# Performance work log

Measured on AMD Instinct MI355X. Metric: run time of the kernel, lower is better.

Reference implementation:

```python
import jax, jax.numpy as jnp
import numpy as np

EPS = 1e-6


def setup_inputs() -> dict:
    key = jax.random.key(0)
    k1, k2, k3 = jax.random.split(key, 3)
    N, D, C = 65536, 512, 1000
    x = jax.random.normal(k1, (N, D), dtype=jnp.float32)
    # learned class centers (rows ~ unit-ish scale like the orthogonal init)
    weight = jax.random.normal(k2, (C, D), dtype=jnp.float32) / np.sqrt(D)
    targets = jax.random.randint(k3, (N,), 0, C)
    return {"x": x, "weight": weight, "targets": targets}


def reference(x, weight, targets):
    # Original computes full [N, C] euclidean distances then gathers only the
    # target entry per row via onehot+nonzero. Mathematically identical (and
    # exact, not an approximation) is gathering the target center per sample
    # and computing its distance directly.
    w_t = weight[targets]                               # [N, D] gather by class
    d = jnp.sqrt(jnp.sum((x - w_t) ** 2, axis=1) + EPS)  # [N]
    return jnp.mean(d)
```

## Files before the change

kernel.cpp:

```cpp
#include <hip/hip_runtime.h>


constexpr int D = 512;
constexpr float EPS = 1e-6f;

__global__ __launch_bounds__(256) void centerloss_kernel(
    const float* __restrict__ x,
    const float* __restrict__ w,
    const int*   __restrict__ targets,
    float* __restrict__ out,
    int n_rows)
{
    const int lane = threadIdx.x & 63;
    const int wave = threadIdx.x >> 6;
    const int wavesPerBlock = blockDim.x >> 6;
    const int globalWave = blockIdx.x * wavesPerBlock + wave;
    const int waveCount = gridDim.x * wavesPerBlock;

    float wsum = 0.0f;

    for (int row = globalWave; row < n_rows; row += waveCount) {
        const int t = targets[row];
        const float4* __restrict__ xr =
            reinterpret_cast<const float4*>(x + (size_t)row * D);
        const float4* __restrict__ wr =
            reinterpret_cast<const float4*>(w + (size_t)t * D);

        float4 xa = xr[lane];
        float4 wa = wr[lane];
        float4 xb = xr[lane + 64];
        float4 wb = wr[lane + 64];

        float acc = 0.0f, d0;
        d0 = xa.x - wa.x; acc = fmaf(d0, d0, acc);
        d0 = xa.y - wa.y; acc = fmaf(d0, d0, acc);
        d0 = xa.z - wa.z; acc = fmaf(d0, d0, acc);
        d0 = xa.w - wa.w; acc = fmaf(d0, d0, acc);
        d0 = xb.x - wb.x; acc = fmaf(d0, d0, acc);
        d0 = xb.y - wb.y; acc = fmaf(d0, d0, acc);
        d0 = xb.z - wb.z; acc = fmaf(d0, d0, acc);
        d0 = xb.w - wb.w; acc = fmaf(d0, d0, acc);

        #pragma unroll
        for (int off = 1; off < 64; off <<= 1)
            acc += __shfl_xor(acc, off, 64);

        wsum += sqrtf(acc + EPS);
    }

    __shared__ float smem[8];
    if (lane == 0) smem[wave] = wsum;
    __syncthreads();

    if (threadIdx.x == 0) {
        float s = 0.0f;
        for (int i = 0; i < wavesPerBlock; ++i) s += smem[i];
        atomicAdd(out, s * (1.0f / (float)n_rows));
    }
}

extern "C" void kernel_launch(void* const* d_in, const int* in_sizes, int n_in,
                              void* d_out, int out_size, void* d_ws, size_t ws_size,
                              hipStream_t stream) {
    const float* x       = (const float*)d_in[0];
    const float* weight  = (const float*)d_in[1];
    const int*   targets = (const int*)d_in[2];
    float* out = (float*)d_out;

    const int n_rows = in_sizes[2];

    hipMemsetAsync(d_out, 0, sizeof(float), stream);

    const int block = 256;
    const int grid  = 2048;
    centerloss_kernel<<<grid, block, 0, stream>>>(x, weight, targets, out, n_rows);
}
```

Before: 206.8 us.

## Process contiguous rows per wave with batched target loads and nontemporal x reads

Each wave now owns a contiguous block of 8 rows, loads their targets with one vector load and broadcasts them via readlane, and processes two rows per iteration so more loads are in flight. Loads of x use nontemporal hints so they bypass cache retention, leaving cache for the weight rows, which are reused. The grid is sized to cover every row exactly once instead of using a fixed grid-stride loop, which increases the block count and the number of atomics.

Measured after the change: 200.1 us. -3.2%, faster.

```diff
diff --git a/kernel.cpp b/kernel.cpp
--- a/kernel.cpp
+++ b/kernel.cpp
@@ -1,61 +1,100 @@
 #include <hip/hip_runtime.h>
 
 
+typedef float f32x4 __attribute__((ext_vector_type(4)));
+
 constexpr int D = 512;
 constexpr float EPS = 1e-6f;
+constexpr int RPW = 8;
+constexpr int WPB = 4;
 
 __global__ __launch_bounds__(256) void centerloss_kernel(
     const float* __restrict__ x,
     const float* __restrict__ w,
     const int*   __restrict__ targets,
     float* __restrict__ out,
-    int n_rows)
+    int n_rows, float inv_n)
 {
     const int lane = threadIdx.x & 63;
     const int wave = threadIdx.x >> 6;
-    const int wavesPerBlock = blockDim.x >> 6;
-    const int globalWave = blockIdx.x * wavesPerBlock + wave;
-    const int waveCount = gridDim.x * wavesPerBlock;
+    const int gw = blockIdx.x * WPB + wave;
+    const long base = (long)gw * RPW;
+
+    int tml = 0;
+    {
+        const long r = base + lane;
+        if (lane < RPW && r < (long)n_rows) tml = targets[r];
+    }
 
     float wsum = 0.0f;
+    const f32x4 fz = {0.f, 0.f, 0.f, 0.f};
 
-    for (int row = globalWave; row < n_rows; row += waveCount) {
-        const int t = targets[row];
-        const float4* __restrict__ xr =
-            reinterpret_cast<const float4*>(x + (size_t)row * D);
-        const float4* __restrict__ wr =
-            reinterpret_cast<const float4*>(w + (size_t)t * D);
+    #pragma unroll
+    for (int k = 0; k < RPW; k += 2) {
+        const long r0 = base + k;
+        const long r1 = base + k + 1;
+        const bool v0 = r0 < (long)n_rows;
+        const bool v1 = r1 < (long)n_rows;
+        const int t0 = __builtin_amdgcn_readlane(tml, k);
+        const int t1 = __builtin_amdgcn_readlane(tml, k + 1);
 
-        float4 xa = xr[lane];
-        float4 wa = wr[lane];
-        float4 xb = xr[lane + 64];
-        float4 wb = wr[lane + 64];
+        const f32x4* __restrict__ xr0 = reinterpret_cast<const f32x4*>(x + r0 * D);
+        const f32x4* __restrict__ xr1 = reinterpret_cast<const f32x4*>(x + r1 * D);
+        const f32x4* __restrict__ wr0 = reinterpret_cast<const f32x4*>(w + (size_t)t0 * D);
+        const f32x4* __restrict__ wr1 = reinterpret_cast<const f32x4*>(w + (size_t)t1 * D);
 
-        float acc = 0.0f, d0;
-        d0 = xa.x - wa.x; acc = fmaf(d0, d0, acc);
-        d0 = xa.y - wa.y; acc = fmaf(d0, d0, acc);
-        d0 = xa.z - wa.z; acc = fmaf(d0, d0, acc);
-        d0 = xa.w - wa.w; acc = fmaf(d0, d0, acc);
-        d0 = xb.x - wb.x; acc = fmaf(d0, d0, acc);
-        d0 = xb.y - wb.y; acc = fmaf(d0, d0, acc);
-        d0 = xb.z - wb.z; acc = fmaf(d0, d0, acc);
-        d0 = xb.w - wb.w; acc = fmaf(d0, d0, acc);
+        f32x4 xa0 = fz, xb0 = fz, wa0 = fz, wb0 = fz;
+        f32x4 xa1 = fz, xb1 = fz, wa1 = fz, wb1 = fz;
+        if (v0) {
+            xa0 = __builtin_nontemporal_load(&xr0[lane]);
+            xb0 = __builtin_nontemporal_load(&xr0[lane + 64]);
+            wa0 = wr0[lane];
+            wb0 = wr0[lane + 64];
+        }
+        if (v1) {
+            xa1 = __builtin_nontemporal_load(&xr1[lane]);
+            xb1 = __builtin_nontemporal_load(&xr1[lane + 64]);
+            wa1 = wr1[lane];
+            wb1 = wr1[lane + 64];
+        }
+
+        float a0 = 0.f, a1 = 0.f, d;
+        d = xa0.x - wa0.x; a0 = fmaf(d, d, a0);
+        d = xa0.y - wa0.y; a0 = fmaf(d, d, a0);
+        d = xa0.z - wa0.z; a0 = fmaf(d, d, a0);
+        d = xa0.w - wa0.w; a0 = fmaf(d, d, a0);
+        d = xb0.x - wb0.x; a0 = fmaf(d, d, a0);
+        d = xb0.y - wb0.y; a0 = fmaf(d, d, a0);
+        d = xb0.z - wb0.z; a0 = fmaf(d, d, a0);
+        d = xb0.w - wb0.w; a0 = fmaf(d, d, a0);
+
+        d = xa1.x - wa1.x; a1 = fmaf(d, d, a1);
+        d = xa1.y - wa1.y; a1 = fmaf(d, d, a1);
+        d = xa1.z - wa1.z; a1 = fmaf(d, d, a1);
+        d = xa1.w - wa1.w; a1 = fmaf(d, d, a1);
+        d = xb1.x - wb1.x; a1 = fmaf(d, d, a1);
+        d = xb1.y - wb1.y; a1 = fmaf(d, d, a1);
+        d = xb1.z - wb1.z; a1 = fmaf(d, d, a1);
+        d = xb1.w - wb1.w; a1 = fmaf(d, d, a1);
 
         #pragma unroll
-        for (int off = 1; off < 64; off <<= 1)
-            acc += __shfl_xor(acc, off, 64);
-
-        wsum += sqrtf(acc + EPS);
+        for (int off = 1; off < 64; off <<= 1) {
+            a0 += __shfl_xor(a0, off, 64);
+            a1 += __shfl_xor(a1, off, 64);
+        }
+        if (v0) wsum += sqrtf(a0 + EPS);
+        if (v1) wsum += sqrtf(a1 + EPS);
     }
 
-    __shared__ float smem[8];
+    __shared__ float smem[WPB];
     if (lane == 0) smem[wave] = wsum;
     __syncthreads();
 
     if (threadIdx.x == 0) {
         float s = 0.0f;
-        for (int i = 0; i < wavesPerBlock; ++i) s += smem[i];
-        atomicAdd(out, s * (1.0f / (float)n_rows));
+        #pragma unroll
+        for (int i = 0; i < WPB; ++i) s += smem[i];
+        atomicAdd(out, s * inv_n);
     }
 }
 
@@ -69,9 +108,10 @@
 
     const int n_rows = in_sizes[2];
 
-    hipMemsetAsync(d_out, 0, sizeof(float), stream);
+    (void)hipMemsetAsync(d_out, 0, sizeof(float), stream);
 
-    const int block = 256;
-    const int grid  = 2048;
-    centerloss_kernel<<<grid, block, 0, stream>>>(x, weight, targets, out, n_rows);
+    const int rowsPerBlock = WPB * RPW;
+    const int grid = (n_rows + rowsPerBlock - 1) / rowsPerBlock;
+    centerloss_kernel<<<grid, 256, 0, stream>>>(x, weight, targets, out,
+                                                n_rows, 1.0f / (float)n_rows);
 }
```

## Bucket rows by target class so each block reuses one center in registers

Applied to the files above, without the earlier changes.

Adds a counting-sort pipeline (count, scan, scatter) that groups row indices by target class. The main kernel then runs one block per class, loads that class's center once into registers, and streams the matching x rows with nontemporal loads while prefetching the next row index. The aim is to remove the repeated per-row gather of weight rows. In exchange it adds three extra launches and a memset, atomic contention on the class counters, and load imbalance across the 1000 class blocks. Reads of x become scattered rather than sequential.

After: 234.0 us. 1.13x slower.

```diff
diff --git a/kernel.cpp b/kernel.cpp
--- a/kernel.cpp
+++ b/kernel.cpp
@@ -1,61 +1,96 @@
 #include <hip/hip_runtime.h>
 
+
+typedef float f32x4 __attribute__((ext_vector_type(4)));
 
 constexpr int D = 512;
 constexpr float EPS = 1e-6f;
 
-__global__ __launch_bounds__(256) void centerloss_kernel(
-    const float* __restrict__ x,
-    const float* __restrict__ w,
-    const int*   __restrict__ targets,
-    float* __restrict__ out,
-    int n_rows)
+__global__ void k_count(const int* __restrict__ targets, int n,
+                        int* __restrict__ counts) {
+    int i = blockIdx.x * blockDim.x + threadIdx.x;
+    if (i < n) atomicAdd(&counts[targets[i]], 1);
+}
+
+__global__ __launch_bounds__(1024) void k_scan(const int* __restrict__ counts,
+                                               int* __restrict__ offsets,
+                                               int* __restrict__ cursors, int C) {
+    __shared__ int s[1024];
+    const int tid = threadIdx.x;
+    const int cnt = (tid < C) ? counts[tid] : 0;
+    s[tid] = cnt;
+    __syncthreads();
+    for (int off = 1; off < 1024; off <<= 1) {
+        int v = (tid >= off) ? s[tid - off] : 0;
+        __syncthreads();
+        s[tid] += v;
+        __syncthreads();
+    }
+    if (tid < C) {
+        const int excl = s[tid] - cnt;
+        offsets[tid] = excl;
+        cursors[tid] = excl;
+    }
+}
+
+__global__ void k_scatter(const int* __restrict__ targets, int n,
+                          int* __restrict__ cursors, int* __restrict__ bucket) {
+    int i = blockIdx.x * blockDim.x + threadIdx.x;
+    if (i < n) {
+        int pos = atomicAdd(&cursors[targets[i]], 1);
+        bucket[pos] = i;
+    }
+}
+
+__global__ __launch_bounds__(256) void k_main(
+    const float* __restrict__ x, const float* __restrict__ w,
+    const int* __restrict__ offsets, const int* __restrict__ counts,
+    const int* __restrict__ bucket, float* __restrict__ out, float inv_n)
 {
     const int lane = threadIdx.x & 63;
     const int wave = threadIdx.x >> 6;
-    const int wavesPerBlock = blockDim.x >> 6;
-    const int globalWave = blockIdx.x * wavesPerBlock + wave;
-    const int waveCount = gridDim.x * wavesPerBlock;
+    const int c = blockIdx.x;
+    const int start = offsets[c];
+    const int cnt   = counts[c];
+
+    const f32x4* __restrict__ wr = reinterpret_cast<const f32x4*>(w + (size_t)c * D);
+    const f32x4 wa = wr[lane];
+    const f32x4 wb = wr[lane + 64];
 
     float wsum = 0.0f;
 
-    for (int row = globalWave; row < n_rows; row += waveCount) {
-        const int t = targets[row];
-        const float4* __restrict__ xr =
-            reinterpret_cast<const float4*>(x + (size_t)row * D);
-        const float4* __restrict__ wr =
-            reinterpret_cast<const float4*>(w + (size_t)t * D);
+    int row = (wave < cnt) ? bucket[start + wave] : 0;
+    for (int j = wave; j < cnt; j += 4) {
+        const int nrow = (j + 4 < cnt) ? bucket[start + j + 4] : 0;
 
-        float4 xa = xr[lane];
-        float4 wa = wr[lane];
-        float4 xb = xr[lane + 64];
-        float4 wb = wr[lane + 64];
+        const f32x4* __restrict__ xr =
+            reinterpret_cast<const f32x4*>(x + (size_t)row * D);
+        const f32x4 xa = __builtin_nontemporal_load(&xr[lane]);
+        const f32x4 xb = __builtin_nontemporal_load(&xr[lane + 64]);
 
-        float acc = 0.0f, d0;
-        d0 = xa.x - wa.x; acc = fmaf(d0, d0, acc);
-        d0 = xa.y - wa.y; acc = fmaf(d0, d0, acc);
-        d0 = xa.z - wa.z; acc = fmaf(d0, d0, acc);
-        d0 = xa.w - wa.w; acc = fmaf(d0, d0, acc);
-        d0 = xb.x - wb.x; acc = fmaf(d0, d0, acc);
-        d0 = xb.y - wb.y; acc = fmaf(d0, d0, acc);
-        d0 = xb.z - wb.z; acc = fmaf(d0, d0, acc);
-        d0 = xb.w - wb.w; acc = fmaf(d0, d0, acc);
+        float a = 0.0f, d;
+        d = xa.x - wa.x; a = fmaf(d, d, a);
+        d = xa.y - wa.y; a = fmaf(d, d, a);
+        d = xa.z - wa.z; a = fmaf(d, d, a);
+        d = xa.w - wa.w; a = fmaf(d, d, a);
+        d = xb.x - wb.x; a = fmaf(d, d, a);
+        d = xb.y - wb.y; a = fmaf(d, d, a);
+        d = xb.z - wb.z; a = fmaf(d, d, a);
+        d = xb.w - wb.w; a = fmaf(d, d, a);
 
         #pragma unroll
         for (int off = 1; off < 64; off <<= 1)
-            acc += __shfl_xor(acc, off, 64);
+            a += __shfl_xor(a, off, 64);
 
-        wsum += sqrtf(acc + EPS);
+        wsum += sqrtf(a + EPS);
+        row = nrow;
     }
 
-    __shared__ float smem[8];
+    __shared__ float smem[4];
     if (lane == 0) smem[wave] = wsum;
     __syncthreads();
-
     if (threadIdx.x == 0) {
-        float s = 0.0f;
-        for (int i = 0; i < wavesPerBlock; ++i) s += smem[i];
-        atomicAdd(out, s * (1.0f / (float)n_rows));
+        atomicAdd(out, (smem[0] + smem[1] + smem[2] + smem[3]) * inv_n);
     }
 }
 
@@ -68,10 +103,22 @@
     float* out = (float*)d_out;
 
     const int n_rows = in_sizes[2];
+    const int C      = in_sizes[1] / D;
 
-    hipMemsetAsync(d_out, 0, sizeof(float), stream);
+    int* ws_i    = (int*)d_ws;
+    int* counts  = ws_i;
+    int* offsets = ws_i + 1024;
+    int* cursors = ws_i + 2048;
+    int* bucket  = ws_i + 3072;
 
-    const int block = 256;
-    const int grid  = 2048;
-    centerloss_kernel<<<grid, block, 0, stream>>>(x, weight, targets, out, n_rows);
+    (void)hipMemsetAsync(d_out, 0, sizeof(float), stream);
+    (void)hipMemsetAsync(counts, 0, 1024 * sizeof(int), stream);
+
+    const int tblk = 256;
+    const int tgrid = (n_rows + tblk - 1) / tblk;
+    k_count  <<<tgrid, tblk, 0, stream>>>(targets, n_rows, counts);
+    k_scan   <<<1, 1024, 0, stream>>>(counts, offsets, cursors, C);
+    k_scatter<<<tgrid, tblk, 0, stream>>>(targets, n_rows, cursors, bucket);
+    k_main   <<<C, 256, 0, stream>>>(x, weight, offsets, counts, bucket,
+                                     out, 1.0f / (float)n_rows);
 }
```

## Process four rows per wave with 16-lane groups and one-shot grid

Applied to the files above, without the earlier changes.

Each wave now owns a fixed chunk of 8 rows and splits into four 16-lane groups, each reducing one row per step with 8 vector loads per lane, so the cross-lane reduction shrinks to 4 shuffle stages. Targets are loaded once per wave and broadcast by shuffle. The grid-stride loop is replaced by one block per 32 rows, giving many more blocks and more loads in flight per lane. Because every lane in a group holds the full row sum, the wave total is 16 times too large, and the final scale divides by 16N to compensate. The cost is more blocks and more atomics on the output.

Result: slower. 213.8 us (+3.4%).

```diff
diff --git a/kernel.cpp b/kernel.cpp
--- a/kernel.cpp
+++ b/kernel.cpp
@@ -1,61 +1,80 @@
 #include <hip/hip_runtime.h>
 
 
+typedef float f32x4 __attribute__((ext_vector_type(4)));
+
 constexpr int D = 512;
 constexpr float EPS = 1e-6f;
+constexpr int RPW = 8;
+constexpr int WPB = 4;
 
 __global__ __launch_bounds__(256) void centerloss_kernel(
     const float* __restrict__ x,
     const float* __restrict__ w,
     const int*   __restrict__ targets,
     float* __restrict__ out,
-    int n_rows)
+    int n_rows, float inv_16n)
 {
     const int lane = threadIdx.x & 63;
     const int wave = threadIdx.x >> 6;
-    const int wavesPerBlock = blockDim.x >> 6;
-    const int globalWave = blockIdx.x * wavesPerBlock + wave;
-    const int waveCount = gridDim.x * wavesPerBlock;
+    const int grp  = lane >> 4;
+    const int sub  = lane & 15;
+    const int gw = blockIdx.x * WPB + wave;
+    const long base = (long)gw * RPW;
+
+    int tml = 0;
+    if (lane < RPW) {
+        const long r = base + lane;
+        if (r < (long)n_rows) tml = targets[r];
+    }
 
     float wsum = 0.0f;
+    const bool fast = (base + RPW) <= (long)n_rows;
 
-    for (int row = globalWave; row < n_rows; row += waveCount) {
-        const int t = targets[row];
-        const float4* __restrict__ xr =
-            reinterpret_cast<const float4*>(x + (size_t)row * D);
-        const float4* __restrict__ wr =
-            reinterpret_cast<const float4*>(w + (size_t)t * D);
+    #pragma unroll
+    for (int step = 0; step < 2; ++step) {
+        const long r = base + step * 4 + grp;
+        const int  t = __shfl(tml, step * 4 + grp, 64);
+        const bool v = fast || (r < (long)n_rows);
 
-        float4 xa = xr[lane];
-        float4 wa = wr[lane];
-        float4 xb = xr[lane + 64];
-        float4 wb = wr[lane + 64];
-
-        float acc = 0.0f, d0;
-        d0 = xa.x - wa.x; acc = fmaf(d0, d0, acc);
-        d0 = xa.y - wa.y; acc = fmaf(d0, d0, acc);
-        d0 = xa.z - wa.z; acc = fmaf(d0, d0, acc);
-        d0 = xa.w - wa.w; acc = fmaf(d0, d0, acc);
-        d0 = xb.x - wb.x; acc = fmaf(d0, d0, acc);
-        d0 = xb.y - wb.y; acc = fmaf(d0, d0, acc);
-        d0 = xb.z - wb.z; acc = fmaf(d0, d0, acc);
-        d0 = xb.w - wb.w; acc = fmaf(d0, d0, acc);
+        float a = 0.0f;
+        if (v) {
+            const f32x4* __restrict__ xr =
+                reinterpret_cast<const f32x4*>(x + r * D);
+            const f32x4* __restrict__ wr =
+                reinterpret_cast<const f32x4*>(w + (size_t)t * D);
+            #pragma unroll
+            for (int j = 0; j < 8; ++j) {
+                const f32x4 xv = xr[sub + j * 16];
+                const f32x4 wv = wr[sub + j * 16];
+                float d;
+                d = xv.x - wv.x; a = fmaf(d, d, a);
+                d = xv.y - wv.y; a = fmaf(d, d, a);
+                d = xv.z - wv.z; a = fmaf(d, d, a);
+                d = xv.w - wv.w; a = fmaf(d, d, a);
+            }
+        }
 
         #pragma unroll
-        for (int off = 1; off < 64; off <<= 1)
-            acc += __shfl_xor(acc, off, 64);
+        for (int off = 1; off < 16; off <<= 1)
+            a += __shfl_xor(a, off, 64);
 
-        wsum += sqrtf(acc + EPS);
+        if (v) wsum += sqrtf(a + EPS);
     }
 
-    __shared__ float smem[8];
+    #pragma unroll
+    for (int off = 1; off < 64; off <<= 1)
+        wsum += __shfl_xor(wsum, off, 64);
+
+    __shared__ float smem[WPB];
     if (lane == 0) smem[wave] = wsum;
     __syncthreads();
 
     if (threadIdx.x == 0) {
         float s = 0.0f;
-        for (int i = 0; i < wavesPerBlock; ++i) s += smem[i];
-        atomicAdd(out, s * (1.0f / (float)n_rows));
+        #pragma unroll
+        for (int i = 0; i < WPB; ++i) s += smem[i];
+        atomicAdd(out, s * inv_16n);
     }
 }
 
@@ -69,9 +88,11 @@
 
     const int n_rows = in_sizes[2];
 
-    hipMemsetAsync(d_out, 0, sizeof(float), stream);
+    (void)hipMemsetAsync(d_out, 0, sizeof(float), stream);
 
-    const int block = 256;
-    const int grid  = 2048;
-    centerloss_kernel<<<grid, block, 0, stream>>>(x, weight, targets, out, n_rows);
+    const int rowsPerBlock = WPB * RPW;
+    const int grid = (n_rows + rowsPerBlock - 1) / rowsPerBlock;
+    centerloss_kernel<<<grid, 256, 0, stream>>>(x, weight, targets, out,
+                                                n_rows,
+                                                1.0f / (16.0f * (float)n_rows));
 }
```
